# Kernel optimization log

Measured on AMD Instinct MI355X. Metric: run time of the kernel, lower is better.

The kernel has to match this reference:

```python
import jax, jax.numpy as jnp
import numpy as np
from jax import lax

B, T, D = 8, 704, 1024
R, K, HD = 16, 4, 64          # num_rules, top_k(rules), head_dim
SD, E = 32, 3                 # select_dim, num_entities
CTX = E // 2                  # entities kept per selected rule = 1
SEG_LENS = np.array([128.0, 64.0, 512.0], np.float32)  # prompt / descriptor / input segments
SEG_LENS_J = jnp.asarray(SEG_LENS)


def _seg_mask():
    m = np.zeros((E, T), np.float32)
    m[0, :128] = 1.0
    m[1, 128:192] = 1.0
    m[2, 192:] = 1.0
    return jnp.asarray(m)


def _ln(x, g, b):
    mu = x.mean(-1, keepdims=True)
    var = ((x - mu) ** 2).mean(-1, keepdims=True)
    return (x - mu) * lax.rsqrt(var + 1e-5) * g + b


def _st_topk(scores, k):
    # hard top-k multi-hot mask with straight-through gradient (TopkArgMax)
    _, idx = lax.top_k(scores, k)
    hard = jax.nn.one_hot(idx, scores.shape[-1], dtype=scores.dtype).sum(-2)
    return hard + scores - lax.stop_gradient(scores)


def setup_inputs() -> dict:
    key = jax.random.key(0)
    ks = jax.random.split(key, 16)
    g = lambda i, shape, s=0.02: jax.random.normal(ks[i], shape, jnp.float32) * s
    return dict(
        hidden_states=jax.random.normal(ks[0], (B, T, D), jnp.float32),
        attention_mask=jnp.zeros((B, T, T), jnp.float32),
        rules_embed=g(1, (K, R, HD), 0.1),
        W_ent=g(2, (D, SD)), b_ent=jnp.zeros((SD,), jnp.float32),
        Wq_er=g(3, (HD, SD)), Wk_er=g(4, (SD, SD)),
        Wq_es=g(5, (K, HD, SD // 2)), Wk_es=g(6, (SD, SD // 2)),
        Wq=g(7, (D, D)), bq=jnp.zeros((D,), jnp.float32),
        Wk=g(8, (D, D)), bk=jnp.zeros((D,), jnp.float32),
        Wv=g(9, (D, D)), bv=jnp.zeros((D,), jnp.float32),
        Wo=g(10, (HD, D)), bo=jnp.zeros((D,), jnp.float32),
        ln1_g=jnp.ones((D,), jnp.float32), ln1_b=jnp.zeros((D,), jnp.float32),
        ln2_g=jnp.ones((D,), jnp.float32), ln2_b=jnp.zeros((D,), jnp.float32),
        fc1_w1=g(11, (D, D // 2)), fc1_w2=g(12, (D // 2, 4 * D)),
        fc2_w1=g(13, (4 * D, D // 2)), fc2_w2=g(14, (D // 2, D)),
    )


def _forward(hidden_states, attention_mask, rules_embed, W_ent, b_ent,
             Wq_er, Wk_er, Wq_es, Wk_es, Wq, bq, Wk, bk, Wv, bv, Wo, bo,
             ln1_g, ln1_b, ln2_g, ln2_b, fc1_w1, fc1_w2, fc2_w1, fc2_w2):
    seg = _seg_mask()                                   # [E,T] entity token masks
    residual = hidden_states
    h = _ln(hidden_states, ln1_g, ln1_b)                # [B,T,D]

    # --- EntityEncoder: masked mean-pool per entity segment -> select_dim
    pooled = jnp.einsum('et,btd->bed', seg, h) / SEG_LENS_J[None, :, None]
    entities = pooled @ W_ent + b_ent                   # [B,E,SD]

    # --- rule/entity selection (eval: hard top-1 over rules x entities)
    q_er = jnp.einsum('krh,hd->krd', rules_embed, Wq_er)           # [K,R,SD] shared query
    k_er = entities @ Wk_er                                        # [B,E,SD]
    s_er = jnp.einsum('krd,bed->bkre', q_er, k_er) / np.float32(np.sqrt(SD))
    mask = _st_topk(s_er.reshape(B, K, R * E), 1)                  # [B,K,R*E]
    rule_mask = mask.reshape(B, K, R, E).sum(-1)                   # [B,K,R]
    selected_rules = jnp.einsum('bkr,krh->bkh', rule_mask, rules_embed)  # [B,K,HD]

    # --- entity selection per selected rule (grouped query, top-ctx_size)
    q_es = jnp.einsum('bkh,khi->bki', selected_rules, Wq_es)
    k_es = entities @ Wk_es                                        # [B,E,SD//2]
    s_es = jnp.einsum('bki,bei->bke', q_es, k_es) / np.float32(np.sqrt(SD // 2))
    entity_mask = _st_topk(s_es, CTX)                              # [B,K,E]

    # --- masked gather-sum over (top_k, entities) without [B,K,E,T,D] blowup
    tok_gate = jnp.einsum('bke,et->bt', entity_mask, seg)          # [B,T]
    hg = h * tok_gate[:, :, None]                                  # [B,T,D]

    # --- per-rule self-attention
    scale = np.float32(HD ** -0.5)
    q = ((hg @ Wq + bq) * scale).reshape(B, T, R, HD).transpose(0, 2, 1, 3)
    kk = (hg @ Wk + bk).reshape(B, T, R, HD).transpose(0, 2, 1, 3)
    v = (hg @ Wv + bv).reshape(B, T, R, HD).transpose(0, 2, 1, 3)
    aw = jnp.einsum('brqh,brkh->brqk', q, kk) + attention_mask[:, None]
    ap = jax.nn.softmax(aw, axis=-1)
    ao = jnp.einsum('brqk,brkh->brqh', ap, v)                      # [B,R,T,HD]

    # --- combine over rules per top-k slot, project, sum over slots
    sel = jnp.einsum('bkr,brth->bkth', rule_mask, ao)              # [B,K,T,HD]
    attn_out = (jnp.einsum('bkth,hd->bktd', sel, Wo) + bo).sum(1)  # [B,T,D] (bias summed K times, as in torch)

    h = residual + attn_out
    residual = h
    x = _ln(h, ln2_g, ln2_b).reshape(B * T, D)
    # GroupMLP (num=1, hidden=D//2) with internal relu; outer activation_fn=gelu
    x = jax.nn.gelu(jax.nn.relu(x @ fc1_w1) @ fc1_w2, approximate=False)
    x = jax.nn.relu(x @ fc2_w1) @ fc2_w2
    return residual + x.reshape(B, T, D)


def reference(hidden_states, attention_mask, rules_embed, W_ent, b_ent,
              Wq_er, Wk_er, Wq_es, Wk_es, Wq, bq, Wk, bk, Wv, bv, Wo, bo,
              ln1_g, ln1_b, ln2_g, ln2_b, fc1_w1, fc1_w2, fc2_w1, fc2_w2):
    return _forward(hidden_states, attention_mask, rules_embed, W_ent, b_ent,
                    Wq_er, Wk_er, Wq_es, Wk_es, Wq, bq, Wk, bk, Wv, bv, Wo, bo,
                    ln1_g, ln1_b, ln2_g, ln2_b, fc1_w1, fc1_w2, fc2_w1, fc2_w2)
```

## Files before the change

kernel.cpp:

```cpp
#include <hip/hip_runtime.h>
#include <hip/hip_bf16.h>
#include <math.h>

#define BB 8
#define TT 704
#define DD 1024
#define RR 16
#define KK 4
#define HDH 64
#define BT (BB*TT)

typedef unsigned short u16;
typedef __attribute__((ext_vector_type(4))) float f32x4;
typedef __attribute__((ext_vector_type(8))) short bf16x8;
typedef __attribute__((ext_vector_type(4))) unsigned short u16x4;
typedef __attribute__((ext_vector_type(8))) unsigned short u16x8;

__device__ __forceinline__ u16 f2bf(float f) {
    union { float f; unsigned int u; } cv; cv.f = f;
    unsigned int u = cv.u;
    unsigned int r = (u + 0x7fffu + ((u >> 16) & 1u)) >> 16;
    return (u16)r;
}

__device__ __forceinline__ float bf2f(u16 v) {
    union { unsigned int u; float f; } cv; cv.u = ((unsigned int)v) << 16;
    return cv.f;
}

__device__ __forceinline__ void gl2lds(const u16* g, u16* l) {
    __builtin_amdgcn_global_load_lds(
        (const __attribute__((address_space(1))) void*)g,
        (__attribute__((address_space(3))) void*)l, 16, 0, 0);
}

template<int N> __device__ __forceinline__ void waitv() {
    if constexpr (N == 0) asm volatile("s_waitcnt vmcnt(0)" ::: "memory");
    else if constexpr (N == 2) asm volatile("s_waitcnt vmcnt(2)" ::: "memory");
    else if constexpr (N == 3) asm volatile("s_waitcnt vmcnt(3)" ::: "memory");
    else asm volatile("s_waitcnt vmcnt(4)" ::: "memory");
}

template<int OBF16, int IBF16>
__global__ __launch_bounds__(256)
void ln_kernel(const void* __restrict__ xv, const float* __restrict__ g,
               const float* __restrict__ be, void* __restrict__ yv)
{
    const int row = blockIdx.x;
    const int tid = threadIdx.x;
    __shared__ float sbuf[4];
    const size_t off = (size_t)row * DD + tid * 4;
    float4 v;
    if (IBF16) {
        u16x4 xb = *(const u16x4*)((const u16*)xv + off);
        v.x = bf2f(xb[0]); v.y = bf2f(xb[1]); v.z = bf2f(xb[2]); v.w = bf2f(xb[3]);
    } else {
        v = *(const float4*)((const float*)xv + off);
    }
    float s = v.x + v.y + v.z + v.w;
#pragma unroll
    for (int o = 32; o; o >>= 1) s += __shfl_xor(s, o);
    if ((tid & 63) == 0) sbuf[tid >> 6] = s;
    __syncthreads();
    float mean = (sbuf[0] + sbuf[1] + sbuf[2] + sbuf[3]) * (1.f / 1024.f);
    float dx = v.x - mean, dy = v.y - mean, dz = v.z - mean, dw = v.w - mean;
    float q = dx*dx + dy*dy + dz*dz + dw*dw;
    __syncthreads();
#pragma unroll
    for (int o = 32; o; o >>= 1) q += __shfl_xor(q, o);
    if ((tid & 63) == 0) sbuf[tid >> 6] = q;
    __syncthreads();
    float var = (sbuf[0] + sbuf[1] + sbuf[2] + sbuf[3]) * (1.f / 1024.f);
    float rstd = rsqrtf(var + 1e-5f);
    float4 gg = *(const float4*)(g + tid * 4);
    float4 bb4 = *(const float4*)(be + tid * 4);
    float o0 = dx * rstd * gg.x + bb4.x;
    float o1 = dy * rstd * gg.y + bb4.y;
    float o2 = dz * rstd * gg.z + bb4.z;
    float o3 = dw * rstd * gg.w + bb4.w;
    if (OBF16) {
        u16x4 o4 = {f2bf(o0), f2bf(o1), f2bf(o2), f2bf(o3)};
        *(u16x4*)((u16*)yv + off) = o4;
    } else {
        float4 o4 = {o0, o1, o2, o3};
        *(float4*)((float*)yv + off) = o4;
    }
}

__global__ __launch_bounds__(256)
void pool_partial_kernel(const float* __restrict__ h, float* __restrict__ partial)
{
    const int chunk = blockIdx.x, b = blockIdx.y;
    const int d = threadIdx.x * 4;
    const float* p = h + ((size_t)b * TT + chunk * 64) * DD + d;
    float4 s = {0.f, 0.f, 0.f, 0.f};
    for (int t = 0; t < 64; ++t) {
        float4 v = *(const float4*)(p + (size_t)t * DD);
        s.x += v.x; s.y += v.y; s.z += v.z; s.w += v.w;
    }
    *(float4*)(partial + ((size_t)(b * 11 + chunk)) * 1024 + d) = s;
}

__global__ __launch_bounds__(256)
void pool_finish_kernel(const float* __restrict__ partial, const float* __restrict__ W_ent,
                        const float* __restrict__ b_ent, float* __restrict__ entities)
{
    const int b = blockIdx.x / 3, e = blockIdx.x % 3;
    const int c0 = (e == 0) ? 0 : (e == 1) ? 2 : 3;
    const int c1 = (e == 0) ? 2 : (e == 1) ? 3 : 11;
    const float invlen = (e == 0) ? (1.f/128.f) : (e == 1) ? (1.f/64.f) : (1.f/512.f);
    __shared__ float pooled[1024];
    __shared__ float part[8][32];
    const int tid = threadIdx.x;
    {
        const int d = tid * 4;
        float4 s = {0.f, 0.f, 0.f, 0.f};
        for (int c = c0; c < c1; ++c) {
            float4 v = *(const float4*)(partial + ((size_t)(b * 11 + c)) * 1024 + d);
            s.x += v.x; s.y += v.y; s.z += v.z; s.w += v.w;
        }
        pooled[d+0] = s.x * invlen; pooled[d+1] = s.y * invlen;
        pooled[d+2] = s.z * invlen; pooled[d+3] = s.w * invlen;
    }
    __syncthreads();
    const int g = tid >> 5, j = tid & 31;
    float s = 0.f;
    for (int d = g * 128; d < g * 128 + 128; ++d) s = fmaf(pooled[d], W_ent[d * 32 + j], s);
    part[g][j] = s;
    __syncthreads();
    if (tid < 32) {
        float s2 = b_ent[tid];
        for (int g2 = 0; g2 < 8; ++g2) s2 += part[g2][tid];
        entities[blockIdx.x * 32 + tid] = s2;
    }
}

__global__ __launch_bounds__(256)
void select_kernel(const float* __restrict__ entities, const float* __restrict__ rules,
                   const float* __restrict__ Wq_er, const float* __restrict__ Wk_er,
                   const float* __restrict__ Wq_es, const float* __restrict__ Wk_es,
                   int* __restrict__ slot_rule, float* __restrict__ gate)
{
    __shared__ float rules_s[4096];
    __shared__ float Wq_er_s[2048];
    __shared__ float Wq_es_s[4096];
    __shared__ float Wk_er_s[1024];
    __shared__ float Wk_es_s[512];
    __shared__ float ent_s[768];
    __shared__ float q_er_s[2048];
    __shared__ float k_er_s[768];
    __shared__ float k_es_s[384];
    __shared__ float qes_s[32][16];
    __shared__ int   rsel_s[32];
    __shared__ int   sel_e[32];
    const int tid = threadIdx.x;
    for (int i = tid; i < 1024; i += 256) *(float4*)&rules_s[i*4] = *(const float4*)&rules[i*4];
    for (int i = tid; i < 512;  i += 256) *(float4*)&Wq_er_s[i*4] = *(const float4*)&Wq_er[i*4];
    for (int i = tid; i < 1024; i += 256) *(float4*)&Wq_es_s[i*4] = *(const float4*)&Wq_es[i*4];
    if (tid < 256) *(float4*)&Wk_er_s[tid*4] = *(const float4*)&Wk_er[tid*4];
    if (tid < 128) *(float4*)&Wk_es_s[tid*4] = *(const float4*)&Wk_es[tid*4];
    if (tid < 192) *(float4*)&ent_s[tid*4] = *(const float4*)&entities[tid*4];
    __syncthreads();
    for (int idx = tid; idx < 2048; idx += 256) {
        int k = idx >> 9, rem = idx & 511, r = rem >> 5, d = rem & 31;
        float s = 0.f;
        for (int hh = 0; hh < 64; ++hh)
            s = fmaf(rules_s[(k * 16 + r) * 64 + hh], Wq_er_s[hh * 32 + d], s);
        q_er_s[idx] = s;
    }
    for (int idx = tid; idx < 768; idx += 256) {
        int be = idx >> 5, d = idx & 31;
        float s = 0.f;
        for (int ss = 0; ss < 32; ++ss)
            s = fmaf(ent_s[be * 32 + ss], Wk_er_s[ss * 32 + d], s);
        k_er_s[idx] = s;
    }
    for (int idx = tid; idx < 384; idx += 256) {
        int be = idx >> 4, i = idx & 15;
        float s = 0.f;
        for (int ss = 0; ss < 32; ++ss)
            s = fmaf(ent_s[be * 32 + ss], Wk_es_s[ss * 16 + i], s);
        k_es_s[idx] = s;
    }
    __syncthreads();
    {
        const int pair = tid >> 3, slice = tid & 7;
        const int b = pair >> 2, k = pair & 3;
        float best = -1e30f; int bj = 48;
        for (int j = slice * 6; j < slice * 6 + 6; ++j) {
            const int r = j / 3, e = j - 3 * r;
            const float* qp = &q_er_s[(k * 16 + r) * 32];
            const float* kp = &k_er_s[(b * 3 + e) * 32];
            float s = 0.f;
            for (int d = 0; d < 32; ++d) s = fmaf(qp[d], kp[d], s);
            s *= 0.17677669529663687f;
            if (s > best) { best = s; bj = j; }
        }
#pragma unroll
        for (int off = 1; off < 8; off <<= 1) {
            float os = __shfl_xor(best, off);
            int oj = __shfl_xor(bj, off);
            if (os > best || (os == best && oj < bj)) { best = os; bj = oj; }
        }
        if (slice == 0) { rsel_s[pair] = bj / 3; slot_rule[pair] = bj / 3; }
    }
    __syncthreads();
    {
        const int pair = tid >> 3, slice = tid & 7;
        const int k = pair & 3, rstar = rsel_s[pair];
#pragma unroll
        for (int ii = 0; ii < 2; ++ii) {
            const int i = slice * 2 + ii;
            float s = 0.f;
            for (int hh = 0; hh < 64; ++hh)
                s = fmaf(rules_s[(k * 16 + rstar) * 64 + hh], Wq_es_s[(k * 64 + hh) * 16 + i], s);
            qes_s[pair][i] = s;
        }
    }
    __syncthreads();
    if ((tid & 7) == 0) {
        const int pair = tid >> 3, b = pair >> 2;
        float best2 = -1e30f; int ei = 0;
        for (int e = 0; e < 3; ++e) {
            float s = 0.f;
            for (int i = 0; i < 16; ++i) s = fmaf(qes_s[pair][i], k_es_s[(b * 3 + e) * 16 + i], s);
            s *= 0.25f;
            if (s > best2) { best2 = s; ei = e; }
        }
        sel_e[pair] = ei;
    }
    __syncthreads();
    if (tid < 24) {
        const int b = tid / 3, e = tid % 3;
        float g = 0.f;
        for (int k = 0; k < 4; ++k) g += (sel_e[b * 4 + k] == e) ? 1.f : 0.f;
        gate[b * 3 + e] = g;
    }
}

__global__ __launch_bounds__(256)
void hg_kernel(const float* __restrict__ h, const float* __restrict__ gate,
               u16* __restrict__ hgb)
{
    const int row = blockIdx.x;
    const int b = row / TT, t = row - b * TT;
    const float g = gate[b * 3 + ((t < 128) ? 0 : (t < 192) ? 1 : 2)];
    const size_t off = (size_t)row * DD + threadIdx.x * 4;
    float4 v = *(const float4*)(h + off);
    u16x4 o = {f2bf(v.x * g), f2bf(v.y * g), f2bf(v.z * g), f2bf(v.w * g)};
    *(u16x4*)(hgb + off) = o;
}

__device__ __forceinline__ void transpose_tile(const float* __restrict__ in,
                                               u16* __restrict__ out,
                                               int R, int C, int tr, int tc)
{
    __shared__ float tile[32][33];
    const int tx = threadIdx.x & 31, ty = threadIdx.x >> 5;
    const int c0 = tc * 32, r0 = tr * 32;
#pragma unroll
    for (int j = 0; j < 4; ++j)
        tile[ty + j * 8][tx] = in[(size_t)(r0 + ty + j * 8) * C + c0 + tx];
    __syncthreads();
#pragma unroll
    for (int j = 0; j < 4; ++j)
        out[(size_t)(c0 + ty + j * 8) * R + r0 + tx] = f2bf(tile[tx][ty + j * 8]);
}

__device__ __forceinline__ void transpose_tile_rep4(const float* __restrict__ in,
                                                    u16* __restrict__ out,
                                                    int tr, int tc)
{
    __shared__ float tile[32][33];
    const int tx = threadIdx.x & 31, ty = threadIdx.x >> 5;
    const int c0 = tc * 32, r0 = tr * 32;
#pragma unroll
    for (int j = 0; j < 4; ++j)
        tile[ty + j * 8][tx] = in[(size_t)(r0 + ty + j * 8) * 1024 + c0 + tx];
    __syncthreads();
#pragma unroll
    for (int j = 0; j < 4; ++j) {
        const u16 v = f2bf(tile[tx][ty + j * 8]);
        u16* o = out + (size_t)(c0 + ty + j * 8) * 256 + r0 + tx;
#pragma unroll
        for (int rep = 0; rep < 4; ++rep) o[rep * 64] = v;
    }
}

__global__ __launch_bounds__(256)
void transpose_batch1_kernel(const float* __restrict__ Wq, const float* __restrict__ Wk,
                             const float* __restrict__ Wv, const float* __restrict__ Wo,
                             const float* __restrict__ fc1w1, const float* __restrict__ fc2w2,
                             u16* __restrict__ WqkvT, u16* __restrict__ WoT4,
                             u16* __restrict__ fc1w1T, u16* __restrict__ fc2w2T)
{
    const int bid = blockIdx.x;
    if (bid < 3072) {
        const int m = bid >> 10, t = bid & 1023;
        const float* in = (m == 0) ? Wq : (m == 1) ? Wk : Wv;
        transpose_tile(in, WqkvT + (size_t)m * 1024 * 1024, 1024, 1024, t >> 5, t & 31);
    } else if (bid < 3136) {
        const int t = bid - 3072;
        transpose_tile_rep4(Wo, WoT4, t >> 5, t & 31);
    } else if (bid < 3648) {
        const int t = bid - 3136;
        transpose_tile(fc1w1, fc1w1T, 1024, 512, t >> 4, t & 15);
    } else {
        const int t = bid - 3648;
        transpose_tile(fc2w2, fc2w2T, 512, 1024, t >> 5, t & 31);
    }
}

__global__ __launch_bounds__(256)
void transpose_batch2_kernel(const float* __restrict__ fc1w2, const float* __restrict__ fc2w1,
                             u16* __restrict__ fc1w2T, u16* __restrict__ fc2w1T)
{
    const int bid = blockIdx.x;
    if (bid < 2048) transpose_tile(fc1w2, fc1w2T, 512, 4096, bid >> 7, bid & 127);
    else { const int t = bid - 2048; transpose_tile(fc2w1, fc2w1T, 4096, 512, t >> 4, t & 15); }
}

template<int BN, int ACT, int OBF16, int RESB>
__global__ __launch_bounds__(256)
void gemm2(const u16* __restrict__ A, int lda, const u16* __restrict__ Bt, int ldb,
           void* C0, void* C1, void* C2, void* C3, int ldc, int M, int Ksub,
           const void* __restrict__ resid, const float* __restrict__ bias, float bscale)
{
    constexpr int MI = (BN == 128) ? 4 : 2;
    constexpr int NLOAD = 2 + ((BN == 128) ? 2 : 1);
    __shared__ u16 As[3][128 * 32];
    __shared__ u16 Bs[3][BN * 32];
    const int tid = threadIdx.x;
    const int wid = tid >> 6, lane = tid & 63;
    const int z = blockIdx.z;
    const int row0 = blockIdx.y * 128, col0 = blockIdx.x * BN;
    const size_t koff = (size_t)z * Ksub;
    const int srA = wid * 32 + (lane >> 2);
    const int sc = (lane & 3) * 8;
    const u16* ag = A + (size_t)(row0 + srA) * lda + koff + sc;
    const int srB = (BN == 128) ? (wid * 32 + (lane >> 2)) : (wid * 16 + (lane >> 2));
    const u16* bg = Bt + (size_t)(col0 + srB) * ldb + koff + sc;
    const int nt = Ksub >> 5;

    auto STAGE = [&](int buf, int t) {
        const u16* a = ag + t * 32;
        const u16* b = bg + t * 32;
        gl2lds(a, &As[buf][wid * 1024]);
        gl2lds(a + (size_t)16 * lda, &As[buf][wid * 1024 + 512]);
        if constexpr (BN == 128) {
            gl2lds(b, &Bs[buf][wid * 1024]);
            gl2lds(b + (size_t)16 * ldb, &Bs[buf][wid * 1024 + 512]);
        } else {
            gl2lds(b, &Bs[buf][wid * 512]);
        }
    };

    f32x4 acc[MI][4];
#pragma unroll
    for (int i = 0; i < MI; ++i)
#pragma unroll
        for (int j = 0; j < 4; ++j) acc[i][j] = (f32x4){0.f, 0.f, 0.f, 0.f};

    const int fr = lane & 15, kb8 = (lane >> 4) * 8;
    const int wrbase = (BN == 128) ? (wid >> 1) * 64 : wid * 32;
    const int wcbase = (BN == 128) ? (wid & 1) * 64 : 0;
    const int paoff = (wrbase + fr) * 32 + kb8;
    const int pboff = (wcbase + fr) * 32 + kb8;

    STAGE(0, 0);
    if (nt > 1) STAGE(1, 1);
    for (int t = 0; t < nt; ++t) {
        if (t + 1 < nt) waitv<NLOAD>(); else waitv<0>();
        __builtin_amdgcn_s_barrier();
        asm volatile("" ::: "memory");
        const int buf = t % 3;
#pragma unroll
        for (int mi = 0; mi < MI; ++mi) {
            bf16x8 af = *(const bf16x8*)&As[buf][paoff + mi * 512];
#pragma unroll
            for (int ni = 0; ni < 4; ++ni) {
                bf16x8 bfv = *(const bf16x8*)&Bs[buf][pboff + ni * 512];
                acc[mi][ni] = __builtin_amdgcn_mfma_f32_16x16x32_bf16(af, bfv, acc[mi][ni], 0, 0, 0);
            }
        }
        if (t + 2 < nt) STAGE((t + 2) % 3, t + 2);
    }

    void* Cp = (z == 0) ? C0 : (z == 1) ? C1 : (z == 2) ? C2 : C3;
    const int fq4 = (lane >> 4) * 4;
#pragma unroll
    for (int mi = 0; mi < MI; ++mi) {
#pragma unroll
        for (int j = 0; j < 4; ++j) {
            const int row = row0 + wrbase + mi * 16 + fq4 + j;
#pragma unroll
            for (int ni = 0; ni < 4; ++ni) {
                const int col = col0 + wcbase + ni * 16 + fr;
                float v = acc[mi][ni][j];
                if (bias) v += bscale * bias[col];
                if (ACT == 1) v = fmaxf(v, 0.f);
                else if (ACT == 2) v = 0.5f * v * (1.f + erff(v * 0.70710678118654752f));
                const size_t off = (size_t)row * ldc + col;
                if (OBF16) {
                    ((u16*)Cp)[off] = f2bf(v);
                } else {
                    if (resid) v += RESB ? bf2f(((const u16*)resid)[off])
                                         : ((const float*)resid)[off];
                    ((float*)Cp)[off] = v;
                }
            }
        }
    }
}

template<int NP>
__global__ __launch_bounds__(256)
void red_relu_kernel(const float* __restrict__ p0, const float* __restrict__ p1,
                     const float* __restrict__ p2, const float* __restrict__ p3,
                     u16* __restrict__ out)
{
    const int i = (blockIdx.x * 256 + threadIdx.x) * 4;
    float4 a = *(const float4*)(p0 + i);
    float4 b = *(const float4*)(p1 + i);
    a.x += b.x; a.y += b.y; a.z += b.z; a.w += b.w;
    if (NP == 4) {
        float4 c = *(const float4*)(p2 + i);
        float4 d = *(const float4*)(p3 + i);
        a.x += c.x + d.x; a.y += c.y + d.y; a.z += c.z + d.z; a.w += c.w + d.w;
    }
    u16x4 o = {f2bf(fmaxf(a.x, 0.f)), f2bf(fmaxf(a.y, 0.f)),
               f2bf(fmaxf(a.z, 0.f)), f2bf(fmaxf(a.w, 0.f))};
    *(u16x4*)(out + i) = o;
}

__global__ __launch_bounds__(256)
void combine_mfma_kernel(const u16* __restrict__ AO, const u16* __restrict__ WoT4,
                         const float* __restrict__ hidden, const float* __restrict__ bo,
                         u16* __restrict__ hmid)
{
    __shared__ u16 As[3][128 * 32];
    __shared__ u16 Bs[3][128 * 32];
    const int tid = threadIdx.x;
    const int wid = tid >> 6, lane = tid & 63;
    const int row0 = blockIdx.y * 128, col0 = blockIdx.x * 128;
    const int srA = wid * 32 + (lane >> 2);
    const int sc = (lane & 3) * 8;
    const int arow0 = row0 + srA, arow1 = arow0 + 16;
    const int ab0 = arow0 / TT, at0 = arow0 - ab0 * TT;
    const int ab1 = arow1 / TT, at1 = arow1 - ab1 * TT;
    const u16* abase0 = AO + ((size_t)(ab0 * 4) * TT + at0) * 64 + sc;
    const u16* abase1 = AO + ((size_t)(ab1 * 4) * TT + at1) * 64 + sc;
    const u16* bg = WoT4 + (size_t)(col0 + srA) * 256 + sc;
    const int nt = 8;

    auto STAGE = [&](int buf, int t) {
        const int k0 = t * 32;
        const size_t delta = (size_t)(k0 >> 6) * (TT * 64) + (k0 & 63);
        gl2lds(abase0 + delta, &As[buf][wid * 1024]);
        gl2lds(abase1 + delta, &As[buf][wid * 1024 + 512]);
        gl2lds(bg + k0, &Bs[buf][wid * 1024]);
        gl2lds(bg + k0 + (size_t)16 * 256, &Bs[buf][wid * 1024 + 512]);
    };

    f32x4 acc[4][4];
#pragma unroll
    for (int i = 0; i < 4; ++i)
#pragma unroll
        for (int j = 0; j < 4; ++j) acc[i][j] = (f32x4){0.f, 0.f, 0.f, 0.f};
    const int fr = lane & 15, kb8 = (lane >> 4) * 8;
    const int wrbase = (wid >> 1) * 64, wcbase = (wid & 1) * 64;
    const int paoff = (wrbase + fr) * 32 + kb8;
    const int pboff = (wcbase + fr) * 32 + kb8;

    STAGE(0, 0);
    STAGE(1, 1);
    for (int t = 0; t < nt; ++t) {
        if (t + 1 < nt) waitv<4>(); else waitv<0>();
        __builtin_amdgcn_s_barrier();
        asm volatile("" ::: "memory");
        const int buf = t % 3;
#pragma unroll
        for (int mi = 0; mi < 4; ++mi) {
            bf16x8 af = *(const bf16x8*)&As[buf][paoff + mi * 512];
#pragma unroll
            for (int ni = 0; ni < 4; ++ni) {
                bf16x8 bfv = *(const bf16x8*)&Bs[buf][pboff + ni * 512];
                acc[mi][ni] = __builtin_amdgcn_mfma_f32_16x16x32_bf16(af, bfv, acc[mi][ni], 0, 0, 0);
            }
        }
        if (t + 2 < nt) STAGE((t + 2) % 3, t + 2);
    }

    const int fq4 = (lane >> 4) * 4;
#pragma unroll
    for (int mi = 0; mi < 4; ++mi)
#pragma unroll
        for (int j = 0; j < 4; ++j) {
            const int row = row0 + wrbase + mi * 16 + fq4 + j;
#pragma unroll
            for (int ni = 0; ni < 4; ++ni) {
                const int col = col0 + wcbase + ni * 16 + fr;
                const size_t off = (size_t)row * DD + col;
                float v = acc[mi][ni][j] + 4.f * bo[col] + hidden[off];
                hmid[off] = f2bf(v);
            }
        }
}

__global__ __launch_bounds__(256)
void qkv3_mfma_kernel(const u16* __restrict__ hgb, const u16* __restrict__ WqkvT,
                      const float* __restrict__ bq, const float* __restrict__ bk,
                      const float* __restrict__ bv, const int* __restrict__ slot_rule,
                      u16* __restrict__ Qb, u16* __restrict__ Kb, u16* __restrict__ VT)
{
    const int z = blockIdx.x, mt = blockIdx.y;
    const int b = z >> 2;
    const int r = slot_rule[z];
    __shared__ u16 As[3][64 * 32];
    __shared__ u16 Bs[3][3][64 * 32];
    const int tid = threadIdx.x;
    const int w = tid >> 6, lane = tid & 63;
    const u16* ag = hgb + ((size_t)b * TT + mt * 64 + (tid >> 2)) * DD + (tid & 3) * 8;
    const u16* bg0 = WqkvT + (size_t)0 * DD * DD + (size_t)(r * 64 + (tid >> 2)) * DD + (tid & 3) * 8;
    const u16* bg1 = WqkvT + (size_t)1 * DD * DD + (size_t)(r * 64 + (tid >> 2)) * DD + (tid & 3) * 8;
    const u16* bg2 = WqkvT + (size_t)2 * DD * DD + (size_t)(r * 64 + (tid >> 2)) * DD + (tid & 3) * 8;
    auto STAGE = [&](int buf, int t) {
        gl2lds(ag  + t * 32, &As[buf][w * 512]);
        gl2lds(bg0 + t * 32, &Bs[buf][0][w * 512]);
        gl2lds(bg1 + t * 32, &Bs[buf][1][w * 512]);
        gl2lds(bg2 + t * 32, &Bs[buf][2][w * 512]);
    };
    f32x4 accq[4], acck[4], accv[4];
#pragma unroll
    for (int i = 0; i < 4; ++i) {
        accq[i] = (f32x4){0.f, 0.f, 0.f, 0.f};
        acck[i] = (f32x4){0.f, 0.f, 0.f, 0.f};
        accv[i] = (f32x4){0.f, 0.f, 0.f, 0.f};
    }
    const int fr = lane & 15, kb8 = (lane >> 4) * 8;
    const int paoff = (w * 16 + fr) * 32 + kb8;
    const int nt = 32;
    STAGE(0, 0);
    STAGE(1, 1);
    for (int t = 0; t < nt; ++t) {
        if (t + 1 < nt) waitv<4>(); else waitv<0>();
        __builtin_amdgcn_s_barrier();
        asm volatile("" ::: "memory");
        const int buf = t % 3;
        bf16x8 af = *(const bf16x8*)&As[buf][paoff];
#pragma unroll
        for (int ni = 0; ni < 4; ++ni) {
            const int boff = (ni * 16 + fr) * 32 + kb8;
            bf16x8 bq8 = *(const bf16x8*)&Bs[buf][0][boff];
            bf16x8 bk8 = *(const bf16x8*)&Bs[buf][1][boff];
            bf16x8 bv8 = *(const bf16x8*)&Bs[buf][2][boff];
            accq[ni] = __builtin_amdgcn_mfma_f32_16x16x32_bf16(af, bq8, accq[ni], 0, 0, 0);
            acck[ni] = __builtin_amdgcn_mfma_f32_16x16x32_bf16(af, bk8, acck[ni], 0, 0, 0);
            accv[ni] = __builtin_amdgcn_mfma_f32_16x16x32_bf16(bv8, af, accv[ni], 0, 0, 0);
        }
        if (t + 2 < nt) STAGE((t + 2) % 3, t + 2);
    }
    const size_t bs = (size_t)z * TT;
    const int fq4 = (lane >> 4) * 4;
#pragma unroll
    for (int ni = 0; ni < 4; ++ni)
#pragma unroll
        for (int j = 0; j < 4; ++j) {
            const int row = mt * 64 + w * 16 + fq4 + j;
            const int col = ni * 16 + fr;
            Qb[(bs + row) * 64 + col] = f2bf((accq[ni][j] + bq[r * 64 + col]) * 0.125f);
            Kb[(bs + row) * 64 + col] = f2bf(acck[ni][j] + bk[r * 64 + col]);
            const int d = ni * 16 + fq4 + j;
            const int tt2 = mt * 64 + w * 16 + fr;
            VT[((size_t)z * 64 + d) * TT + tt2] = f2bf(accv[ni][j] + bv[r * 64 + d]);
        }
}

__global__ __launch_bounds__(256)
void attn_mfma_kernel(const u16* __restrict__ Qb, const u16* __restrict__ Kb,
                      const u16* __restrict__ VT, const float* __restrict__ amask,
                      u16* __restrict__ AO)
{
    const int slot = blockIdx.x, qt = blockIdx.y, b = blockIdx.z;
    const int z = b * 4 + slot;
    const size_t bs = (size_t)z * TT;
    const int tid = threadIdx.x;
    const int w = tid >> 6, lane = tid & 63;
    const int fr = lane & 15, g = lane >> 4;
    const int q0 = qt * 64 + w * 16;

    __shared__ u16 Ks[64 * 72];
    __shared__ u16 VTs[64 * 72];
    __shared__ u16 Ps[4][16 * 72];

    bf16x8 qa[2];
    qa[0] = *(const bf16x8*)(Qb + (bs + q0 + fr) * 64 + g * 8);
    qa[1] = *(const bf16x8*)(Qb + (bs + q0 + fr) * 64 + 32 + g * 8);

    float m_run[4], l_run[4];
    f32x4 oacc[4];
#pragma unroll
    for (int j = 0; j < 4; ++j) { m_run[j] = -1e30f; l_run[j] = 0.f; }
#pragma unroll
    for (int ni = 0; ni < 4; ++ni) oacc[ni] = (f32x4){0.f, 0.f, 0.f, 0.f};

    const float* mrow = amask + ((size_t)b * TT + q0 + g * 4) * TT;

    for (int kc = 0; kc < 11; ++kc) {
        const int kv0 = kc * 64;
        __syncthreads();
#pragma unroll
        for (int it = 0; it < 2; ++it) {
            const int idx = tid + it * 256;
            const int row = idx >> 3, ch = (idx & 7) * 8;
            *(u16x8*)&Ks[row * 72 + ch]  = *(const u16x8*)(Kb + (bs + kv0 + row) * 64 + ch);
            *(u16x8*)&VTs[row * 72 + ch] = *(const u16x8*)(VT + ((size_t)z * 64 + row) * TT + kv0 + ch);
        }
        __syncthreads();
        f32x4 sacc[4];
#pragma unroll
        for (int ni = 0; ni < 4; ++ni) sacc[ni] = (f32x4){0.f, 0.f, 0.f, 0.f};
#pragma unroll
        for (int c = 0; c < 2; ++c)
#pragma unroll
            for (int ni = 0; ni < 4; ++ni) {
                bf16x8 bf = *(const bf16x8*)&Ks[(ni * 16 + fr) * 72 + c * 32 + g * 8];
                sacc[ni] = __builtin_amdgcn_mfma_f32_16x16x32_bf16(qa[c], bf, sacc[ni], 0, 0, 0);
            }
        float mloc[4] = {-1e30f, -1e30f, -1e30f, -1e30f};
#pragma unroll
        for (int ni = 0; ni < 4; ++ni)
#pragma unroll
            for (int j = 0; j < 4; ++j) {
                float s = sacc[ni][j] + mrow[(size_t)j * TT + kv0 + ni * 16 + fr];
                sacc[ni][j] = s;
                mloc[j] = fmaxf(mloc[j], s);
            }
#pragma unroll
        for (int o = 1; o < 16; o <<= 1)
#pragma unroll
            for (int j = 0; j < 4; ++j) mloc[j] = fmaxf(mloc[j], __shfl_xor(mloc[j], o));
        float fac[4], lsum[4];
#pragma unroll
        for (int j = 0; j < 4; ++j) {
            const float mn = fmaxf(m_run[j], mloc[j]);
            fac[j] = __expf(m_run[j] - mn);
            m_run[j] = mn;
            lsum[j] = 0.f;
        }
#pragma unroll
        for (int ni = 0; ni < 4; ++ni)
#pragma unroll
            for (int j = 0; j < 4; ++j) {
                const float p = __expf(sacc[ni][j] - m_run[j]);
                lsum[j] += p;
                Ps[w][(g * 4 + j) * 72 + ni * 16 + fr] = f2bf(p);
            }
#pragma unroll
        for (int o = 1; o < 16; o <<= 1)
#pragma unroll
            for (int j = 0; j < 4; ++j) lsum[j] += __shfl_xor(lsum[j], o);
#pragma unroll
        for (int j = 0; j < 4; ++j) l_run[j] = l_run[j] * fac[j] + lsum[j];
#pragma unroll
        for (int ni = 0; ni < 4; ++ni)
#pragma unroll
            for (int j = 0; j < 4; ++j) oacc[ni][j] *= fac[j];
#pragma unroll
        for (int c = 0; c < 2; ++c) {
            bf16x8 paf = *(const bf16x8*)&Ps[w][fr * 72 + c * 32 + g * 8];
#pragma unroll
            for (int ni = 0; ni < 4; ++ni) {
                bf16x8 vf = *(const bf16x8*)&VTs[(ni * 16 + fr) * 72 + c * 32 + g * 8];
                oacc[ni] = __builtin_amdgcn_mfma_f32_16x16x32_bf16(paf, vf, oacc[ni], 0, 0, 0);
            }
        }
    }
#pragma unroll
    for (int j = 0; j < 4; ++j) {
        const float inv = 1.f / l_run[j];
        const int t = q0 + g * 4 + j;
#pragma unroll
        for (int ni = 0; ni < 4; ++ni)
            AO[(bs + t) * 64 + ni * 16 + fr] = f2bf(oacc[ni][j] * inv);
    }
}

extern "C" void kernel_launch(void* const* d_in, const int* in_sizes, int n_in,
                              void* d_out, int out_size, void* d_ws, size_t ws_size,
                              hipStream_t stream)
{
    const float* hidden = (const float*)d_in[0];
    const float* amask  = (const float*)d_in[1];
    const float* rules  = (const float*)d_in[2];
    const float* W_ent  = (const float*)d_in[3];
    const float* b_ent  = (const float*)d_in[4];
    const float* Wq_er  = (const float*)d_in[5];
    const float* Wk_er  = (const float*)d_in[6];
    const float* Wq_es  = (const float*)d_in[7];
    const float* Wk_es  = (const float*)d_in[8];
    const float* Wq     = (const float*)d_in[9];
    const float* bq     = (const float*)d_in[10];
    const float* Wk     = (const float*)d_in[11];
    const float* bk     = (const float*)d_in[12];
    const float* Wv     = (const float*)d_in[13];
    const float* bv     = (const float*)d_in[14];
    const float* Wo     = (const float*)d_in[15];
    const float* bo     = (const float*)d_in[16];
    const float* ln1_g  = (const float*)d_in[17];
    const float* ln1_b  = (const float*)d_in[18];
    const float* ln2_g  = (const float*)d_in[19];
    const float* ln2_b  = (const float*)d_in[20];
    const float* fc1_w1 = (const float*)d_in[21];
    const float* fc1_w2 = (const float*)d_in[22];
    const float* fc2_w1 = (const float*)d_in[23];
    const float* fc2_w2 = (const float*)d_in[24];

    char* ws = (char*)d_ws;
    float* h      = (float*)(ws + 0);
    u16*   x1     = (u16*)(ws + 0);
    u16*   x3b    = (u16*)(ws + 5767168);
    float* g3p1   = (float*)(ws + 11534336);
    float* g3p2   = (float*)(ws + 17301504);
    u16*   hmid   = (u16*)(ws + 23068672);
    float* g3p3   = (float*)(ws + 34603008);
    u16*   hgb    = (u16*)(ws + 46137344);
    u16*   xln2   = (u16*)(ws + 46137344);
    u16*   x2h    = (u16*)(ws + 46137344);
    u16*   Qb     = (u16*)(ws + 57671680);
    u16*   Kb     = (u16*)(ws + 60555264);
    u16*   VT     = (u16*)(ws + 66322432);
    u16*   AO     = (u16*)(ws + 69206016);
    float* part   = (float*)(ws + 69206016);
    float* g3p0   = (float*)(ws + 74973184);
    float* ent    = (float*)(ws + 80740352);
    float* gate   = (float*)(ws + 80743424);
    int*   srule  = (int*)(ws + 80743552);
    u16*   WqkvT  = (u16*)(ws + 80743680);
    u16*   fc1w2T = (u16*)(ws + 80743680);
    u16*   fc2w1T = (u16*)(ws + 84937984);
    u16*   WoT4   = (u16*)(ws + 89132288);
    u16*   fc1w1T = (u16*)(ws + 89656576);
    u16*   fc2w2T = (u16*)(ws + 90705152);
    float* out    = (float*)d_out;

    ln_kernel<0, 0><<<BT, 256, 0, stream>>>(hidden, ln1_g, ln1_b, h);
    pool_partial_kernel<<<dim3(11, 8), 256, 0, stream>>>(h, part);
    pool_finish_kernel<<<24, 256, 0, stream>>>(part, W_ent, b_ent, ent);
    select_kernel<<<1, 256, 0, stream>>>(ent, rules, Wq_er, Wk_er, Wq_es, Wk_es, srule, gate);
    hg_kernel<<<BT, 256, 0, stream>>>(h, gate, hgb);

    transpose_batch1_kernel<<<4160, 256, 0, stream>>>(Wq, Wk, Wv, Wo, fc1_w1, fc2_w2,
                                                      WqkvT, WoT4, fc1w1T, fc2w2T);

    qkv3_mfma_kernel<<<dim3(32, 11), 256, 0, stream>>>(hgb, WqkvT, bq, bk, bv, srule,
                                                       Qb, Kb, VT);
    transpose_batch2_kernel<<<4096, 256, 0, stream>>>(fc1_w2, fc2_w1, fc1w2T, fc2w1T);

    attn_mfma_kernel<<<dim3(4, 11, 8), 256, 0, stream>>>(Qb, Kb, VT, amask, AO);

    combine_mfma_kernel<<<dim3(8, 44), 256, 0, stream>>>(AO, WoT4, hidden, bo, hmid);

    ln_kernel<1, 1><<<BT, 256, 0, stream>>>(hmid, ln2_g, ln2_b, xln2);

    gemm2<64, 1, 1, 0><<<dim3(8, 44, 1), 256, 0, stream>>>(
        xln2, 1024, fc1w1T, 1024, x1, nullptr, nullptr, nullptr, 512, BT, 1024,
        nullptr, nullptr, 0.f);

    for (int half = 0; half < 2; ++half) {
        const u16* x1h = x1 + (size_t)half * 2816 * 512;
        u16* x3bh = x3b + (size_t)half * 2816 * 512;
        gemm2<128, 2, 1, 0><<<dim3(32, 22, 1), 256, 0, stream>>>(
            x1h, 512, fc1w2T, 512, x2h, nullptr, nullptr, nullptr, 4096, 2816, 512,
            nullptr, nullptr, 0.f);
        gemm2<64, 0, 0, 0><<<dim3(8, 22, 4), 256, 0, stream>>>(
            x2h, 4096, fc2w1T, 4096, g3p0, g3p1, g3p2, g3p3, 512, 2816, 1024,
            nullptr, nullptr, 0.f);
        red_relu_kernel<4><<<1408, 256, 0, stream>>>(g3p0, g3p1, g3p2, g3p3, x3bh);
    }

    gemm2<64, 0, 0, 1><<<dim3(16, 44, 1), 256, 0, stream>>>(
        x3b, 512, fc2w2T, 512, out, nullptr, nullptr, nullptr, 1024, BT, 512,
        hmid, nullptr, 0.f);
}
```

Measured before the change: 290.2 us.

## Fold gate into QKV epilogue, dual-output LN1, XCD swizzle grids, halve split-K

Removes the separate gating kernel: LN1 writes fp32 and bf16 outputs in one pass, and the per-segment gate is applied inside the QKV GEMM epilogue as a scalar on the accumulators. Most GEMM and attention launches become 1D grids, with block ids remapped so neighbouring tiles land on the same XCD, aiming at better L2 locality. The fc2_w1 GEMM moves from 4-way to 2-way split-K, so there are fewer fp32 partial buffers to write and reduce, at the cost of fewer blocks in flight. The gate is applied to the fp32 accumulator instead of the bf16-rounded input, which changes rounding slightly.

Measured after the change: 270.0 us. -7.0%, faster.

```diff
diff --git a/kernel.cpp b/kernel.cpp
--- a/kernel.cpp
+++ b/kernel.cpp
@@ -39,6 +39,10 @@
     else if constexpr (N == 2) asm volatile("s_waitcnt vmcnt(2)" ::: "memory");
     else if constexpr (N == 3) asm volatile("s_waitcnt vmcnt(3)" ::: "memory");
     else asm volatile("s_waitcnt vmcnt(4)" ::: "memory");
+}
+
+__device__ __forceinline__ int xcd_swz(int d, int nwg) {
+    return (d & 7) * (nwg >> 3) + (d >> 3);
 }
 
 template<int OBF16, int IBF16>
@@ -85,6 +89,43 @@
         float4 o4 = {o0, o1, o2, o3};
         *(float4*)((float*)yv + off) = o4;
     }
+}
+
+__global__ __launch_bounds__(256)
+void ln1_dual_kernel(const float* __restrict__ x, const float* __restrict__ g,
+                     const float* __restrict__ be, float* __restrict__ y,
+                     u16* __restrict__ yb)
+{
+    const int row = blockIdx.x;
+    const int tid = threadIdx.x;
+    __shared__ float sbuf[4];
+    const size_t off = (size_t)row * DD + tid * 4;
+    float4 v = *(const float4*)(x + off);
+    float s = v.x + v.y + v.z + v.w;
+#pragma unroll
+    for (int o = 32; o; o >>= 1) s += __shfl_xor(s, o);
+    if ((tid & 63) == 0) sbuf[tid >> 6] = s;
+    __syncthreads();
+    float mean = (sbuf[0] + sbuf[1] + sbuf[2] + sbuf[3]) * (1.f / 1024.f);
+    float dx = v.x - mean, dy = v.y - mean, dz = v.z - mean, dw = v.w - mean;
+    float q = dx*dx + dy*dy + dz*dz + dw*dw;
+    __syncthreads();
+#pragma unroll
+    for (int o = 32; o; o >>= 1) q += __shfl_xor(q, o);
+    if ((tid & 63) == 0) sbuf[tid >> 6] = q;
+    __syncthreads();
+    float var = (sbuf[0] + sbuf[1] + sbuf[2] + sbuf[3]) * (1.f / 1024.f);
+    float rstd = rsqrtf(var + 1e-5f);
+    float4 gg = *(const float4*)(g + tid * 4);
+    float4 bb4 = *(const float4*)(be + tid * 4);
+    float o0 = dx * rstd * gg.x + bb4.x;
+    float o1 = dy * rstd * gg.y + bb4.y;
+    float o2 = dz * rstd * gg.z + bb4.z;
+    float o3 = dw * rstd * gg.w + bb4.w;
+    float4 o4 = {o0, o1, o2, o3};
+    *(float4*)(y + off) = o4;
+    u16x4 ob = {f2bf(o0), f2bf(o1), f2bf(o2), f2bf(o3)};
+    *(u16x4*)(yb + off) = ob;
 }
 
 __global__ __launch_bounds__(256)
@@ -238,19 +279,6 @@
     }
 }
 
-__global__ __launch_bounds__(256)
-void hg_kernel(const float* __restrict__ h, const float* __restrict__ gate,
-               u16* __restrict__ hgb)
-{
-    const int row = blockIdx.x;
-    const int b = row / TT, t = row - b * TT;
-    const float g = gate[b * 3 + ((t < 128) ? 0 : (t < 192) ? 1 : 2)];
-    const size_t off = (size_t)row * DD + threadIdx.x * 4;
-    float4 v = *(const float4*)(h + off);
-    u16x4 o = {f2bf(v.x * g), f2bf(v.y * g), f2bf(v.z * g), f2bf(v.w * g)};
-    *(u16x4*)(hgb + off) = o;
-}
-
 __device__ __forceinline__ void transpose_tile(const float* __restrict__ in,
                                                u16* __restrict__ out,
                                                int R, int C, int tr, int tc)
@@ -320,11 +348,12 @@
     else { const int t = bid - 2048; transpose_tile(fc2w1, fc2w1T, 4096, 512, t >> 4, t & 15); }
 }
 
-template<int BN, int ACT, int OBF16, int RESB>
+template<int BN, int ACT, int OBF16, int RESB, int SWZ>
 __global__ __launch_bounds__(256)
 void gemm2(const u16* __restrict__ A, int lda, const u16* __restrict__ Bt, int ldb,
-           void* C0, void* C1, void* C2, void* C3, int ldc, int M, int Ksub,
-           const void* __restrict__ resid, const float* __restrict__ bias, float bscale)
+           void* C0, void* C1, int ldc, int M, int Ksub,
+           const void* __restrict__ resid, const float* __restrict__ bias, float bscale,
+           int gx, int gy)
 {
     constexpr int MI = (BN == 128) ? 4 : 2;
     constexpr int NLOAD = 2 + ((BN == 128) ? 2 : 1);
@@ -332,8 +361,12 @@
     __shared__ u16 Bs[3][BN * 32];
     const int tid = threadIdx.x;
     const int wid = tid >> 6, lane = tid & 63;
-    const int z = blockIdx.z;
-    const int row0 = blockIdx.y * 128, col0 = blockIdx.x * BN;
+    const int bid = SWZ ? xcd_swz(blockIdx.x, gridDim.x) : (int)blockIdx.x;
+    const int col = bid % gx;
+    const int rem = bid / gx;
+    const int row = rem % gy;
+    const int z = rem / gy;
+    const int row0 = row * 128, col0 = col * BN;
     const size_t koff = (size_t)z * Ksub;
     const int srA = wid * 32 + (lane >> 2);
     const int sc = (lane & 3) * 8;
@@ -386,21 +419,21 @@
         if (t + 2 < nt) STAGE((t + 2) % 3, t + 2);
     }
 
-    void* Cp = (z == 0) ? C0 : (z == 1) ? C1 : (z == 2) ? C2 : C3;
+    void* Cp = (z == 0) ? C0 : C1;
     const int fq4 = (lane >> 4) * 4;
 #pragma unroll
     for (int mi = 0; mi < MI; ++mi) {
 #pragma unroll
         for (int j = 0; j < 4; ++j) {
-            const int row = row0 + wrbase + mi * 16 + fq4 + j;
+            const int rw = row0 + wrbase + mi * 16 + fq4 + j;
 #pragma unroll
             for (int ni = 0; ni < 4; ++ni) {
-                const int col = col0 + wcbase + ni * 16 + fr;
+                const int cl = col0 + wcbase + ni * 16 + fr;
                 float v = acc[mi][ni][j];
-                if (bias) v += bscale * bias[col];
+                if (bias) v += bscale * bias[cl];
                 if (ACT == 1) v = fmaxf(v, 0.f);
                 else if (ACT == 2) v = 0.5f * v * (1.f + erff(v * 0.70710678118654752f));
-                const size_t off = (size_t)row * ldc + col;
+                const size_t off = (size_t)rw * ldc + cl;
                 if (OBF16) {
                     ((u16*)Cp)[off] = f2bf(v);
                 } else {
@@ -442,7 +475,8 @@
     __shared__ u16 Bs[3][128 * 32];
     const int tid = threadIdx.x;
     const int wid = tid >> 6, lane = tid & 63;
-    const int row0 = blockIdx.y * 128, col0 = blockIdx.x * 128;
+    const int bid = xcd_swz(blockIdx.x, gridDim.x);
+    const int row0 = (bid >> 3) * 128, col0 = (bid & 7) * 128;
     const int srA = wid * 32 + (lane >> 2);
     const int sc = (lane & 3) * 8;
     const int arow0 = row0 + srA, arow1 = arow0 + 16;
@@ -496,31 +530,36 @@
     for (int mi = 0; mi < 4; ++mi)
 #pragma unroll
         for (int j = 0; j < 4; ++j) {
-            const int row = row0 + wrbase + mi * 16 + fq4 + j;
+            const int rw = row0 + wrbase + mi * 16 + fq4 + j;
 #pragma unroll
             for (int ni = 0; ni < 4; ++ni) {
-                const int col = col0 + wcbase + ni * 16 + fr;
-                const size_t off = (size_t)row * DD + col;
-                float v = acc[mi][ni][j] + 4.f * bo[col] + hidden[off];
+                const int cl = col0 + wcbase + ni * 16 + fr;
+                const size_t off = (size_t)rw * DD + cl;
+                float v = acc[mi][ni][j] + 4.f * bo[cl] + hidden[off];
                 hmid[off] = f2bf(v);
             }
         }
 }
 
 __global__ __launch_bounds__(256)
-void qkv3_mfma_kernel(const u16* __restrict__ hgb, const u16* __restrict__ WqkvT,
+void qkv3_mfma_kernel(const u16* __restrict__ hb, const u16* __restrict__ WqkvT,
                       const float* __restrict__ bq, const float* __restrict__ bk,
                       const float* __restrict__ bv, const int* __restrict__ slot_rule,
+                      const float* __restrict__ gatep,
                       u16* __restrict__ Qb, u16* __restrict__ Kb, u16* __restrict__ VT)
 {
-    const int z = blockIdx.x, mt = blockIdx.y;
-    const int b = z >> 2;
+    const int bid = xcd_swz(blockIdx.x, gridDim.x);
+    const int slot = bid & 3;
+    const int mt = (bid >> 2) % 11;
+    const int b = (bid >> 2) / 11;
+    const int z = b * 4 + slot;
     const int r = slot_rule[z];
+    const float gv = gatep[b * 3 + ((mt < 2) ? 0 : (mt < 3) ? 1 : 2)];
     __shared__ u16 As[3][64 * 32];
     __shared__ u16 Bs[3][3][64 * 32];
     const int tid = threadIdx.x;
     const int w = tid >> 6, lane = tid & 63;
-    const u16* ag = hgb + ((size_t)b * TT + mt * 64 + (tid >> 2)) * DD + (tid & 3) * 8;
+    const u16* ag = hb + ((size_t)b * TT + mt * 64 + (tid >> 2)) * DD + (tid & 3) * 8;
     const u16* bg0 = WqkvT + (size_t)0 * DD * DD + (size_t)(r * 64 + (tid >> 2)) * DD + (tid & 3) * 8;
     const u16* bg1 = WqkvT + (size_t)1 * DD * DD + (size_t)(r * 64 + (tid >> 2)) * DD + (tid & 3) * 8;
     const u16* bg2 = WqkvT + (size_t)2 * DD * DD + (size_t)(r * 64 + (tid >> 2)) * DD + (tid & 3) * 8;
@@ -568,11 +607,11 @@
         for (int j = 0; j < 4; ++j) {
             const int row = mt * 64 + w * 16 + fq4 + j;
             const int col = ni * 16 + fr;
-            Qb[(bs + row) * 64 + col] = f2bf((accq[ni][j] + bq[r * 64 + col]) * 0.125f);
-            Kb[(bs + row) * 64 + col] = f2bf(acck[ni][j] + bk[r * 64 + col]);
+            Qb[(bs + row) * 64 + col] = f2bf((gv * accq[ni][j] + bq[r * 64 + col]) * 0.125f);
+            Kb[(bs + row) * 64 + col] = f2bf(gv * acck[ni][j] + bk[r * 64 + col]);
             const int d = ni * 16 + fq4 + j;
             const int tt2 = mt * 64 + w * 16 + fr;
-            VT[((size_t)z * 64 + d) * TT + tt2] = f2bf(accv[ni][j] + bv[r * 64 + d]);
+            VT[((size_t)z * 64 + d) * TT + tt2] = f2bf(gv * accv[ni][j] + bv[r * 64 + d]);
         }
 }
 
@@ -581,7 +620,10 @@
                       const u16* __restrict__ VT, const float* __restrict__ amask,
                       u16* __restrict__ AO)
 {
-    const int slot = blockIdx.x, qt = blockIdx.y, b = blockIdx.z;
+    const int bid = xcd_swz(blockIdx.x, gridDim.x);
+    const int slot = bid & 3;
+    const int qt = (bid >> 2) % 11;
+    const int b = (bid >> 2) / 11;
     const int z = b * 4 + slot;
     const size_t bs = (size_t)z * TT;
     const int tid = threadIdx.x;
@@ -721,10 +763,8 @@
     u16*   x1     = (u16*)(ws + 0);
     u16*   x3b    = (u16*)(ws + 5767168);
     float* g3p1   = (float*)(ws + 11534336);
-    float* g3p2   = (float*)(ws + 17301504);
     u16*   hmid   = (u16*)(ws + 23068672);
-    float* g3p3   = (float*)(ws + 34603008);
-    u16*   hgb    = (u16*)(ws + 46137344);
+    u16*   hb     = (u16*)(ws + 46137344);
     u16*   xln2   = (u16*)(ws + 46137344);
     u16*   x2h    = (u16*)(ws + 46137344);
     u16*   Qb     = (u16*)(ws + 57671680);
@@ -744,42 +784,41 @@
     u16*   fc2w2T = (u16*)(ws + 90705152);
     float* out    = (float*)d_out;
 
-    ln_kernel<0, 0><<<BT, 256, 0, stream>>>(hidden, ln1_g, ln1_b, h);
+    ln1_dual_kernel<<<BT, 256, 0, stream>>>(hidden, ln1_g, ln1_b, h, hb);
     pool_partial_kernel<<<dim3(11, 8), 256, 0, stream>>>(h, part);
     pool_finish_kernel<<<24, 256, 0, stream>>>(part, W_ent, b_ent, ent);
     select_kernel<<<1, 256, 0, stream>>>(ent, rules, Wq_er, Wk_er, Wq_es, Wk_es, srule, gate);
-    hg_kernel<<<BT, 256, 0, stream>>>(h, gate, hgb);
 
     transpose_batch1_kernel<<<4160, 256, 0, stream>>>(Wq, Wk, Wv, Wo, fc1_w1, fc2_w2,
                                                       WqkvT, WoT4, fc1w1T, fc2w2T);
 
-    qkv3_mfma_kernel<<<dim3(32, 11), 256, 0, stream>>>(hgb, WqkvT, bq, bk, bv, srule,
-                                                       Qb, Kb, VT);
+    qkv3_mfma_kernel<<<352, 256, 0, stream>>>(hb, WqkvT, bq, bk, bv, srule, gate,
+                                              Qb, Kb, VT);
     transpose_batch2_kernel<<<4096, 256, 0, stream>>>(fc1_w2, fc2_w1, fc1w2T, fc2w1T);
 
-    attn_mfma_kernel<<<dim3(4, 11, 8), 256, 0, stream>>>(Qb, Kb, VT, amask, AO);
-
-    combine_mfma_kernel<<<dim3(8, 44), 256, 0, stream>>>(AO, WoT4, hidden, bo, hmid);
+    attn_mfma_kernel<<<352, 256, 0, stream>>>(Qb, Kb, VT, amask, AO);
+
+    combine_mfma_kernel<<<352, 256, 0, stream>>>(AO, WoT4, hidden, bo, hmid);
 
     ln_kernel<1, 1><<<BT, 256, 0, stream>>>(hmid, ln2_g, ln2_b, xln2);
 
-    gemm2<64, 1, 1, 0><<<dim3(8, 44, 1), 256, 0, stream>>>(
-        xln2, 1024, fc1w1T, 1024, x1, nullptr, nullptr, nullptr, 512, BT, 1024,
-        nullptr, nullptr, 0.f);
+    gemm2<64, 1, 1, 0, 1><<<352, 256, 0, stream>>>(
+        xln2, 1024, fc1w1T, 1024, x1, nullptr, 512, BT, 1024,
+        nullptr, nullptr, 0.f, 8, 44);
 
     for (int half = 0; half < 2; ++half) {
         const u16* x1h = x1 + (size_t)half * 2816 * 512;
         u16* x3bh = x3b + (size_t)half * 2816 * 512;
-        gemm2<128, 2, 1, 0><<<dim3(32, 22, 1), 256, 0, stream>>>(
-            x1h, 512, fc1w2T, 512, x2h, nullptr, nullptr, nullptr, 4096, 2816, 512,
-            nullptr, nullptr, 0.f);
-        gemm2<64, 0, 0, 0><<<dim3(8, 22, 4), 256, 0, stream>>>(
-            x2h, 4096, fc2w1T, 4096, g3p0, g3p1, g3p2, g3p3, 512, 2816, 1024,
-            nullptr, nullptr, 0.f);
-        red_relu_kernel<4><<<1408, 256, 0, stream>>>(g3p0, g3p1, g3p2, g3p3, x3bh);
-    }
-
-    gemm2<64, 0, 0, 1><<<dim3(16, 44, 1), 256, 0, stream>>>(
-        x3b, 512, fc2w2T, 512, out, nullptr, nullptr, nullptr, 1024, BT, 512,
-        hmid, nullptr, 0.f);
-}
+        gemm2<128, 2, 1, 0, 0><<<704, 256, 0, stream>>>(
+            x1h, 512, fc1w2T, 512, x2h, nullptr, 4096, 2816, 512,
+            nullptr, nullptr, 0.f, 32, 22);
+        gemm2<64, 0, 0, 0, 1><<<352, 256, 0, stream>>>(
+            x2h, 4096, fc2w1T, 4096, g3p0, g3p1, 512, 2816, 2048,
+            nullptr, nullptr, 0.f, 8, 22);
+        red_relu_kernel<2><<<1408, 256, 0, stream>>>(g3p0, g3p1, nullptr, nullptr, x3bh);
+    }
+
+    gemm2<64, 0, 0, 1, 1><<<704, 256, 0, stream>>>(
+        x3b, 512, fc2w2T, 512, out, nullptr, 1024, BT, 512,
+        hmid, nullptr, 0.f, 16, 44);
+}
```
